# Optimization experiments

Measured on AMD Instinct MI355X. Metric: run time of the kernel, lower is better.

The kernel has to match this reference:

```python
import jax, jax.numpy as jnp
import numpy as np

KERNEL = 3
DILATIONS = (2, 3)
NUM_HEADS = 8


def _unfold_windows(t, k, dil):
    # t: [B, C, H, W] -> [B, C, k*k, H, W], same layout as nn.Unfold(k, dil, pad=dil*(k-1)//2)
    B, C, H, W = t.shape
    pad = dil * (k - 1) // 2
    tp = jnp.pad(t, ((0, 0), (0, 0), (pad, pad), (pad, pad)))
    ws = [tp[:, :, i * dil:i * dil + H, j * dil:j * dil + W]
          for i in range(k) for j in range(k)]
    return jnp.stack(ws, axis=2)


def _dilate_attention(q, k_, v, kernel, dil, head_dim):
    # q,k_,v: [B, d, H, W]
    B, d, H, W = q.shape
    nh = d // head_dim
    scale = head_dim ** (-0.5)
    qh = q.reshape(B, nh, head_dim, H, W)
    kw = _unfold_windows(k_, kernel, dil).reshape(B, nh, head_dim, kernel * kernel, H, W)
    vw = _unfold_windows(v, kernel, dil).reshape(B, nh, head_dim, kernel * kernel, H, W)
    attn = jax.nn.softmax(jnp.einsum('bndhw,bndkhw->bnkhw', qh, kw) * scale, axis=2)
    out = jnp.einsum('bnkhw,bndkhw->bndhw', attn, vw)  # [B, nh, hd, H, W]
    return out.transpose(0, 3, 4, 1, 2).reshape(B, H, W, d)


def setup_inputs() -> dict:
    key = jax.random.key(0)
    k1, k2, k3, k4 = jax.random.split(key, 4)
    B, H, W, C = 4, 128, 128, 256
    x = jax.random.normal(k1, (B, H, W, C), dtype=jnp.float32)
    Wqkv = jax.random.normal(k2, (3 * C, C), dtype=jnp.float32) * (C ** -0.5)
    Wproj = jax.random.normal(k3, (C, C), dtype=jnp.float32) * (C ** -0.5)
    bproj = jnp.zeros((C,), dtype=jnp.float32)
    return {"x": x, "Wqkv": Wqkv, "Wproj": Wproj, "bproj": bproj}


def reference(x, Wqkv, Wproj, bproj):
    B, H, W, C = x.shape
    nd = len(DILATIONS)
    head_dim = C // NUM_HEADS
    # 1x1 conv qkv (no bias), then split into 3 and nd dilation groups
    qkv = jnp.einsum('bhwc,oc->bohw', x, Wqkv).reshape(B, 3, nd, C // nd, H, W)
    outs = []
    for i, dil in enumerate(DILATIONS):
        q, k_, v = qkv[:, 0, i], qkv[:, 1, i], qkv[:, 2, i]
        outs.append(_dilate_attention(q, k_, v, KERNEL, dil, head_dim))
    xo = jnp.concatenate(outs, axis=-1)  # [B, H, W, C], dilation-group-major channels
    return jnp.einsum('bhwc,oc->bhwo', xo, Wproj) + bproj
```

## Files before the change

kernel.cpp:

```cpp
#include <hip/hip_runtime.h>
#include <stdint.h>


typedef __attribute__((ext_vector_type(8))) short bf16x8;
typedef __attribute__((ext_vector_type(4))) float f32x4;

__device__ __forceinline__ void unpack2(unsigned u, float& lo, float& hi) {
  union { unsigned u; float f; } a, b;
  a.u = u << 16;
  b.u = u & 0xffff0000u;
  lo = a.f; hi = b.f;
}
__device__ __forceinline__ unsigned short f2bf(float f) {
  union { float f; unsigned u; } x; x.f = f;
  unsigned r = x.u + 0x7fffu + ((x.u >> 16) & 1u);
  return (unsigned short)(r >> 16);
}
__device__ __forceinline__ unsigned pk2bf(float a, float b) {
  return (unsigned)f2bf(a) | ((unsigned)f2bf(b) << 16);
}

__global__ __launch_bounds__(256) void cvt_f32_to_bf16(
    const float* __restrict__ src, unsigned short* __restrict__ dst, int n) {
  int i = (blockIdx.x * 256 + threadIdx.x) * 8;
  if (i + 8 <= n) {
    const float4* s = (const float4*)(src + i);
    float4 a = s[0], b = s[1];
    uint4 o;
    o.x = pk2bf(a.x, a.y); o.y = pk2bf(a.z, a.w);
    o.z = pk2bf(b.x, b.y); o.w = pk2bf(b.z, b.w);
    *(uint4*)(dst + i) = o;
  } else {
    for (; i < n; ++i) dst[i] = f2bf(src[i]);
  }
}

#define BARX()                                                \
  do {                                                        \
    asm volatile("s_waitcnt lgkmcnt(0)" ::: "memory");        \
    __builtin_amdgcn_s_barrier();                             \
    __builtin_amdgcn_sched_barrier(0);                        \
  } while (0)
#define WAITVM(n)                                             \
  do {                                                        \
    asm volatile("s_waitcnt vmcnt(" #n ")" ::: "memory");     \
    __builtin_amdgcn_sched_barrier(0);                        \
  } while (0)

template <int OUTF32>
__global__ __launch_bounds__(256) void gemm_bt(
    const unsigned short* __restrict__ A, const unsigned short* __restrict__ B,
    void* __restrict__ Cout, const float* __restrict__ bias,
    int N, int NT) {
  __shared__ __align__(16) unsigned short lds[17408];

  const int tid  = threadIdx.x;
  const int lane = tid & 63;
  const int wv   = tid >> 6;
  const int wr   = wv >> 1;
  const int wc   = wv & 1;

  const int nwg = gridDim.x;
  const int q8  = nwg >> 3;
  const int nid = (blockIdx.x & 7) * q8 + (blockIdx.x >> 3);
  const int n0  = (nid % NT) * 128;
  const int m0  = (nid / NT) * 128;

  const int stg_row = wv * 16 + (lane >> 2);
  const int stg_k   = ((lane & 3) ^ ((lane >> 3) & 3)) * 8;
  const unsigned short* Ag = A + (size_t)(m0 + stg_row) * 256 + stg_k;
  const unsigned short* Bg = B + (size_t)(n0 + stg_row) * 256 + stg_k;

  f32x4 acc[4][4];
#pragma unroll
  for (int i = 0; i < 4; ++i)
#pragma unroll
    for (int j = 0; j < 4; ++j) acc[i][j] = (f32x4){0.f, 0.f, 0.f, 0.f};

  const int a_r = lane & 15;

#define STAGE(buf, kt)                                                         \
  do {                                                                         \
    const unsigned short* Asrc = Ag + (kt) * 32;                               \
    const unsigned short* Bsrc = Bg + (kt) * 32;                               \
    _Pragma("unroll")                                                          \
    for (int it = 0; it < 2; ++it) {                                           \
      __builtin_amdgcn_global_load_lds(                                        \
          (const __attribute__((address_space(1))) void*)(Asrc + (size_t)it * 64 * 256), \
          (__attribute__((address_space(3))) void*)&lds[(buf) * 8192 + it * 2048 + wv * 512], \
          16, 0, 0);                                                           \
      __builtin_amdgcn_global_load_lds(                                        \
          (const __attribute__((address_space(1))) void*)(Bsrc + (size_t)it * 64 * 256), \
          (__attribute__((address_space(3))) void*)&lds[(buf) * 8192 + 4096 + it * 2048 + wv * 512], \
          16, 0, 0);                                                           \
    }                                                                          \
  } while (0)

#define COMPUTE(buf)                                                           \
  do {                                                                         \
    const int gsw = (((lane >> 4) ^ ((lane >> 1) & 3))) * 8;                   \
    bf16x8 af[4], bfr[4];                                                      \
    _Pragma("unroll")                                                          \
    for (int mi = 0; mi < 4; ++mi)                                             \
      af[mi] = *(const bf16x8*)&lds[(buf) * 8192 + (wr * 64 + mi * 16 + a_r) * 32 + gsw]; \
    _Pragma("unroll")                                                          \
    for (int ni = 0; ni < 4; ++ni)                                             \
      bfr[ni] = *(const bf16x8*)&lds[(buf) * 8192 + 4096 + (wc * 64 + ni * 16 + a_r) * 32 + gsw]; \
    _Pragma("unroll")                                                          \
    for (int mi = 0; mi < 4; ++mi)                                             \
      _Pragma("unroll")                                                        \
      for (int ni = 0; ni < 4; ++ni)                                           \
        acc[mi][ni] = __builtin_amdgcn_mfma_f32_16x16x32_bf16(                 \
            af[mi], bfr[ni], acc[mi][ni], 0, 0, 0);                            \
  } while (0)

  STAGE(0, 0);
  STAGE(1, 1);
  WAITVM(4);  BARX();
  COMPUTE(0);  BARX();
  STAGE(0, 2); WAITVM(4); BARX();
  COMPUTE(1);  BARX();
  STAGE(1, 3); WAITVM(4); BARX();
  COMPUTE(0);  BARX();
  STAGE(0, 4); WAITVM(4); BARX();
  COMPUTE(1);  BARX();
  STAGE(1, 5); WAITVM(4); BARX();
  COMPUTE(0);  BARX();
  STAGE(0, 6); WAITVM(4); BARX();
  COMPUTE(1);  BARX();
  STAGE(1, 7); WAITVM(4); BARX();
  COMPUTE(0);  BARX();
  WAITVM(0);   BARX();
  COMPUTE(1);  BARX();

  const int cl = wc * 64 + a_r;
  const int rl = wr * 64 + (lane >> 4) * 4;
  if (!OUTF32) {
    unsigned short* eb = &lds[0];
#pragma unroll
    for (int ni = 0; ni < 4; ++ni)
#pragma unroll
      for (int mi = 0; mi < 4; ++mi)
#pragma unroll
        for (int r = 0; r < 4; ++r)
          eb[(rl + mi * 16 + r) * 136 + cl + ni * 16] = f2bf(acc[mi][ni][r]);
    BARX();
    unsigned short* C = (unsigned short*)Cout;
#pragma unroll
    for (int p = 0; p < 8; ++p) {
      const int idx = p * 256 + tid;
      const int row = idx >> 4;
      const int seg = idx & 15;
      uint4 v = *(const uint4*)&eb[row * 136 + seg * 8];
      *(uint4*)&C[(size_t)(m0 + row) * N + n0 + seg * 8] = v;
    }
  } else {
    float* ef = (float*)&lds[0];
    float* C = (float*)Cout;
    float bv[4];
#pragma unroll
    for (int ni = 0; ni < 4; ++ni) bv[ni] = bias[n0 + wc * 64 + ni * 16 + a_r];
#pragma unroll
    for (int half = 0; half < 2; ++half) {
      if (wr == half) {
        const int rb = (lane >> 4) * 4;
#pragma unroll
        for (int ni = 0; ni < 4; ++ni)
#pragma unroll
          for (int mi = 0; mi < 4; ++mi)
#pragma unroll
            for (int r = 0; r < 4; ++r)
              ef[(rb + mi * 16 + r) * 132 + wc * 64 + ni * 16 + a_r] =
                  acc[mi][ni][r] + bv[ni];
      }
      BARX();
#pragma unroll
      for (int p = 0; p < 8; ++p) {
        const int idx = p * 256 + tid;
        const int row = idx >> 5;
        const int seg = idx & 31;
        f32x4 v = *(const f32x4*)&ef[row * 132 + seg * 4];
        *(f32x4*)&C[(size_t)(m0 + half * 64 + row) * N + n0 + seg * 4] = v;
      }
      BARX();
    }
  }
#undef STAGE
#undef COMPUTE
}

__global__ __launch_bounds__(256) void attn_kernel(
    const unsigned short* __restrict__ qkv, unsigned short* __restrict__ xo) {
  const int nwg = gridDim.x;
  const int q8  = nwg >> 3;
  const int bid = (blockIdx.x & 7) * q8 + (blockIdx.x >> 3);
  const int gid   = bid * 256 + threadIdx.x;
  const int combo = gid & 7;
  const int pixel = gid >> 3;
  const int w = pixel & 127;
  const int h = (pixel >> 7) & 127;
  const int b = pixel >> 14;
  const int dil = (combo >> 2) ? 3 : 2;
  const int choff = combo * 32;

  const unsigned short* qp = qkv + (size_t)pixel * 768 + choff;
  float q[32];
#pragma unroll
  for (int t = 0; t < 4; ++t) {
    uint4 u = *(const uint4*)(qp + t * 8);
    unpack2(u.x, q[t * 8 + 0], q[t * 8 + 1]);
    unpack2(u.y, q[t * 8 + 2], q[t * 8 + 3]);
    unpack2(u.z, q[t * 8 + 4], q[t * 8 + 5]);
    unpack2(u.w, q[t * 8 + 6], q[t * 8 + 7]);
  }

  float sc[9];
#pragma unroll
  for (int i = 0; i < 3; ++i) {
#pragma unroll
    for (int j = 0; j < 3; ++j) {
      const int hh = h + (i - 1) * dil;
      const int ww = w + (j - 1) * dil;
      float s = 0.f;
      if ((unsigned)hh < 128u && (unsigned)ww < 128u) {
        const unsigned short* kp =
            qkv + (size_t)((((b << 7) | hh) << 7) | ww) * 768 + 256 + choff;
#pragma unroll
        for (int t = 0; t < 4; ++t) {
          uint4 u = *(const uint4*)(kp + t * 8);
          float a0, a1;
          unpack2(u.x, a0, a1); s += q[t * 8 + 0] * a0 + q[t * 8 + 1] * a1;
          unpack2(u.y, a0, a1); s += q[t * 8 + 2] * a0 + q[t * 8 + 3] * a1;
          unpack2(u.z, a0, a1); s += q[t * 8 + 4] * a0 + q[t * 8 + 5] * a1;
          unpack2(u.w, a0, a1); s += q[t * 8 + 6] * a0 + q[t * 8 + 7] * a1;
        }
      }
      sc[i * 3 + j] = s * 0.17677669529663687f;
    }
  }

  float mx = sc[0];
#pragma unroll
  for (int t = 1; t < 9; ++t) mx = fmaxf(mx, sc[t]);
  float wgt[9], sum = 0.f;
#pragma unroll
  for (int t = 0; t < 9; ++t) { wgt[t] = __expf(sc[t] - mx); sum += wgt[t]; }
  const float inv = 1.f / sum;

  float o[32];
#pragma unroll
  for (int t = 0; t < 32; ++t) o[t] = 0.f;
#pragma unroll
  for (int i = 0; i < 3; ++i) {
#pragma unroll
    for (int j = 0; j < 3; ++j) {
      const int hh = h + (i - 1) * dil;
      const int ww = w + (j - 1) * dil;
      if ((unsigned)hh < 128u && (unsigned)ww < 128u) {
        const float wv = wgt[i * 3 + j] * inv;
        const unsigned short* vp =
            qkv + (size_t)((((b << 7) | hh) << 7) | ww) * 768 + 512 + choff;
#pragma unroll
        for (int t = 0; t < 4; ++t) {
          uint4 u = *(const uint4*)(vp + t * 8);
          float a0, a1;
          unpack2(u.x, a0, a1); o[t * 8 + 0] += wv * a0; o[t * 8 + 1] += wv * a1;
          unpack2(u.y, a0, a1); o[t * 8 + 2] += wv * a0; o[t * 8 + 3] += wv * a1;
          unpack2(u.z, a0, a1); o[t * 8 + 4] += wv * a0; o[t * 8 + 5] += wv * a1;
          unpack2(u.w, a0, a1); o[t * 8 + 6] += wv * a0; o[t * 8 + 7] += wv * a1;
        }
      }
    }
  }

  unsigned short* op = xo + (size_t)pixel * 256 + choff;
#pragma unroll
  for (int t = 0; t < 4; ++t) {
    uint4 u;
    u.x = pk2bf(o[t * 8 + 0], o[t * 8 + 1]);
    u.y = pk2bf(o[t * 8 + 2], o[t * 8 + 3]);
    u.z = pk2bf(o[t * 8 + 4], o[t * 8 + 5]);
    u.w = pk2bf(o[t * 8 + 6], o[t * 8 + 7]);
    *(uint4*)(op + t * 8) = u;
  }
}

extern "C" void kernel_launch(void* const* d_in, const int* in_sizes, int n_in,
                              void* d_out, int out_size, void* d_ws, size_t ws_size,
                              hipStream_t stream) {
  const float* x     = (const float*)d_in[0];
  const float* Wqkv  = (const float*)d_in[1];
  const float* Wproj = (const float*)d_in[2];
  const float* bproj = (const float*)d_in[3];

  const int M = 4 * 128 * 128;
  const int C = 256;

  unsigned short* xb     = (unsigned short*)d_ws;
  unsigned short* qkvb   = xb + (size_t)M * C;
  unsigned short* xob    = qkvb + (size_t)M * 3 * C;
  unsigned short* wqkvb  = xob + (size_t)M * C;
  unsigned short* wprojb = wqkvb + (size_t)3 * C * C;

  cvt_f32_to_bf16<<<(M * C / 8 + 255) / 256, 256, 0, stream>>>(x, xb, M * C);
  cvt_f32_to_bf16<<<(3 * C * C / 8 + 255) / 256, 256, 0, stream>>>(Wqkv, wqkvb, 3 * C * C);
  cvt_f32_to_bf16<<<(C * C / 8 + 255) / 256, 256, 0, stream>>>(Wproj, wprojb, C * C);

  gemm_bt<0><<<(M / 128) * (3 * C / 128), 256, 0, stream>>>(
      xb, wqkvb, (void*)qkvb, nullptr, 3 * C, 3 * C / 128);

  attn_kernel<<<(M * 8) / 256, 256, 0, stream>>>(qkvb, xob);

  gemm_bt<1><<<(M / 128) * (C / 128), 256, 0, stream>>>(
      xob, wprojb, d_out, bproj, C, C / 128);
}
```

Baseline: 130.0 us.

## Tile attention kernel spatially and stage K/V halo in shared memory

The attention kernel now gives each workgroup a 16x16 pixel tile for one head/dilation combo. It cooperatively loads the K and V halo region (22x22 pixels, 8 planes of 8 bf16) into LDS with zero padding, then reads all 9 neighbours from LDS instead of issuing redundant global loads. It also folds the softmax scale into q and uses packed float2 arithmetic. This cuts repeated global/L2 traffic for overlapping windows, at the cost of about 62KB of LDS per block, which limits occupancy, plus a barrier.

```diff
diff --git a/kernel.cpp b/kernel.cpp
--- a/kernel.cpp
+++ b/kernel.cpp
@@ -4,12 +4,13 @@
 
 typedef __attribute__((ext_vector_type(8))) short bf16x8;
 typedef __attribute__((ext_vector_type(4))) float f32x4;
-
-__device__ __forceinline__ void unpack2(unsigned u, float& lo, float& hi) {
+typedef __attribute__((ext_vector_type(2))) float f32x2;
+
+__device__ __forceinline__ f32x2 up2(unsigned u) {
   union { unsigned u; float f; } a, b;
   a.u = u << 16;
   b.u = u & 0xffff0000u;
-  lo = a.f; hi = b.f;
+  return (f32x2){a.f, b.f};
 }
 __device__ __forceinline__ unsigned short f2bf(float f) {
   union { float f; unsigned u; } x; x.f = f;
@@ -191,27 +192,59 @@
 
 __global__ __launch_bounds__(256) void attn_kernel(
     const unsigned short* __restrict__ qkv, unsigned short* __restrict__ xo) {
+  __shared__ __align__(16) unsigned short lds[8 * 485 * 8];
+
   const int nwg = gridDim.x;
   const int q8  = nwg >> 3;
-  const int bid = (blockIdx.x & 7) * q8 + (blockIdx.x >> 3);
-  const int gid   = bid * 256 + threadIdx.x;
-  const int combo = gid & 7;
-  const int pixel = gid >> 3;
-  const int w = pixel & 127;
-  const int h = (pixel >> 7) & 127;
-  const int b = pixel >> 14;
-  const int dil = (combo >> 2) ? 3 : 2;
+  const int nid = (blockIdx.x & 7) * q8 + (blockIdx.x >> 3);
+  const int combo = nid & 7;
+  const int tw    = (nid >> 3) & 7;
+  const int th    = (nid >> 6) & 7;
+  const int b     = nid >> 9;
+  const int d     = (combo >> 2) ? 3 : 2;
   const int choff = combo * 32;
-
-  const unsigned short* qp = qkv + (size_t)pixel * 768 + choff;
-  float q[32];
-#pragma unroll
-  for (int t = 0; t < 4; ++t) {
-    uint4 u = *(const uint4*)(qp + t * 8);
-    unpack2(u.x, q[t * 8 + 0], q[t * 8 + 1]);
-    unpack2(u.y, q[t * 8 + 2], q[t * 8 + 3]);
-    unpack2(u.z, q[t * 8 + 4], q[t * 8 + 5]);
-    unpack2(u.w, q[t * 8 + 6], q[t * 8 + 7]);
+  const int h0 = th * 16, w0 = tw * 16;
+  const int t = threadIdx.x;
+
+#pragma unroll
+  for (int it = 0; it < 16; ++it) {
+    const int slot  = it * 256 + t;
+    const int px    = slot >> 3;
+    const int plane = slot & 7;
+    const int r = px / 22, c = px % 22;
+    const int gh = h0 - d + r;
+    const int gw = w0 - d + c;
+    const bool live = (slot < 3872);
+    const bool ok = live && ((unsigned)gh < 128u) && ((unsigned)gw < 128u);
+    const int hcl = min(max(gh, 0), 127);
+    const int wcl = min(max(gw, 0), 127);
+    const int gp = (((b << 7) | hcl) << 7) | wcl;
+    const unsigned short* src = qkv + (size_t)gp * 768 + 256 +
+                                (plane >> 2) * 256 + (plane & 3) * 8 + choff;
+    uint4 u = *(const uint4*)src;
+    if (!ok) u = make_uint4(0u, 0u, 0u, 0u);
+    if (live) *(uint4*)&lds[(plane * 485 + px) * 8] = u;
+  }
+  __syncthreads();
+
+  const int ph = t >> 4, pw = t & 15;
+  const int gp0 = (((b << 7) | (h0 + ph)) << 7) | (w0 + pw);
+  const unsigned short* qp = qkv + (size_t)gp0 * 768 + choff;
+  f32x2 q2[16];
+  {
+    uint4 u0 = *(const uint4*)qp;
+    uint4 u1 = *(const uint4*)(qp + 8);
+    uint4 u2 = *(const uint4*)(qp + 16);
+    uint4 u3 = *(const uint4*)(qp + 24);
+    const f32x2 s2 = {0.17677669529663687f, 0.17677669529663687f};
+    q2[0]  = up2(u0.x) * s2; q2[1]  = up2(u0.y) * s2;
+    q2[2]  = up2(u0.z) * s2; q2[3]  = up2(u0.w) * s2;
+    q2[4]  = up2(u1.x) * s2; q2[5]  = up2(u1.y) * s2;
+    q2[6]  = up2(u1.z) * s2; q2[7]  = up2(u1.w) * s2;
+    q2[8]  = up2(u2.x) * s2; q2[9]  = up2(u2.y) * s2;
+    q2[10] = up2(u2.z) * s2; q2[11] = up2(u2.w) * s2;
+    q2[12] = up2(u3.x) * s2; q2[13] = up2(u3.y) * s2;
+    q2[14] = up2(u3.z) * s2; q2[15] = up2(u3.w) * s2;
   }
 
   float sc[9];
@@ -219,70 +252,71 @@
   for (int i = 0; i < 3; ++i) {
 #pragma unroll
     for (int j = 0; j < 3; ++j) {
-      const int hh = h + (i - 1) * dil;
-      const int ww = w + (j - 1) * dil;
-      float s = 0.f;
-      if ((unsigned)hh < 128u && (unsigned)ww < 128u) {
-        const unsigned short* kp =
-            qkv + (size_t)((((b << 7) | hh) << 7) | ww) * 768 + 256 + choff;
-#pragma unroll
-        for (int t = 0; t < 4; ++t) {
-          uint4 u = *(const uint4*)(kp + t * 8);
-          float a0, a1;
-          unpack2(u.x, a0, a1); s += q[t * 8 + 0] * a0 + q[t * 8 + 1] * a1;
-          unpack2(u.y, a0, a1); s += q[t * 8 + 2] * a0 + q[t * 8 + 3] * a1;
-          unpack2(u.z, a0, a1); s += q[t * 8 + 4] * a0 + q[t * 8 + 5] * a1;
-          unpack2(u.w, a0, a1); s += q[t * 8 + 6] * a0 + q[t * 8 + 7] * a1;
-        }
-      }
-      sc[i * 3 + j] = s * 0.17677669529663687f;
+      const int lp = (ph + i * d) * 22 + (pw + j * d);
+      const uint4 k0 = *(const uint4*)&lds[(0 * 485 + lp) * 8];
+      const uint4 k1 = *(const uint4*)&lds[(1 * 485 + lp) * 8];
+      const uint4 k2 = *(const uint4*)&lds[(2 * 485 + lp) * 8];
+      const uint4 k3 = *(const uint4*)&lds[(3 * 485 + lp) * 8];
+      f32x2 p0 = q2[0] * up2(k0.x);
+      p0 += q2[1] * up2(k0.y); p0 += q2[2] * up2(k0.z); p0 += q2[3] * up2(k0.w);
+      f32x2 p1 = q2[4] * up2(k1.x);
+      p1 += q2[5] * up2(k1.y); p1 += q2[6] * up2(k1.z); p1 += q2[7] * up2(k1.w);
+      f32x2 p2 = q2[8] * up2(k2.x);
+      p2 += q2[9] * up2(k2.y); p2 += q2[10] * up2(k2.z); p2 += q2[11] * up2(k2.w);
+      f32x2 p3 = q2[12] * up2(k3.x);
+      p3 += q2[13] * up2(k3.y); p3 += q2[14] * up2(k3.z); p3 += q2[15] * up2(k3.w);
+      const f32x2 s = (p0 + p1) + (p2 + p3);
+      sc[i * 3 + j] = s.x + s.y;
     }
   }
 
   float mx = sc[0];
 #pragma unroll
-  for (int t = 1; t < 9; ++t) mx = fmaxf(mx, sc[t]);
-  float wgt[9], sum = 0.f;
-#pragma unroll
-  for (int t = 0; t < 9; ++t) { wgt[t] = __expf(sc[t] - mx); sum += wgt[t]; }
+  for (int k = 1; k < 9; ++k) mx = fmaxf(mx, sc[k]);
+  float sum = 0.f;
+#pragma unroll
+  for (int k = 0; k < 9; ++k) { sc[k] = __expf(sc[k] - mx); sum += sc[k]; }
   const float inv = 1.f / sum;
 
-  float o[32];
-#pragma unroll
-  for (int t = 0; t < 32; ++t) o[t] = 0.f;
+  f32x2 o2[16];
+#pragma unroll
+  for (int k = 0; k < 16; ++k) o2[k] = (f32x2){0.f, 0.f};
 #pragma unroll
   for (int i = 0; i < 3; ++i) {
 #pragma unroll
     for (int j = 0; j < 3; ++j) {
-      const int hh = h + (i - 1) * dil;
-      const int ww = w + (j - 1) * dil;
-      if ((unsigned)hh < 128u && (unsigned)ww < 128u) {
-        const float wv = wgt[i * 3 + j] * inv;
-        const unsigned short* vp =
-            qkv + (size_t)((((b << 7) | hh) << 7) | ww) * 768 + 512 + choff;
-#pragma unroll
-        for (int t = 0; t < 4; ++t) {
-          uint4 u = *(const uint4*)(vp + t * 8);
-          float a0, a1;
-          unpack2(u.x, a0, a1); o[t * 8 + 0] += wv * a0; o[t * 8 + 1] += wv * a1;
-          unpack2(u.y, a0, a1); o[t * 8 + 2] += wv * a0; o[t * 8 + 3] += wv * a1;
-          unpack2(u.z, a0, a1); o[t * 8 + 4] += wv * a0; o[t * 8 + 5] += wv * a1;
-          unpack2(u.w, a0, a1); o[t * 8 + 6] += wv * a0; o[t * 8 + 7] += wv * a1;
-        }
-      }
+      const int lp = (ph + i * d) * 22 + (pw + j * d);
+      const uint4 v0 = *(const uint4*)&lds[(4 * 485 + lp) * 8];
+      const uint4 v1 = *(const uint4*)&lds[(5 * 485 + lp) * 8];
+      const uint4 v2 = *(const uint4*)&lds[(6 * 485 + lp) * 8];
+      const uint4 v3 = *(const uint4*)&lds[(7 * 485 + lp) * 8];
+      const float wv = sc[i * 3 + j] * inv;
+      const f32x2 w2 = {wv, wv};
+      o2[0]  += w2 * up2(v0.x); o2[1]  += w2 * up2(v0.y);
+      o2[2]  += w2 * up2(v0.z); o2[3]  += w2 * up2(v0.w);
+      o2[4]  += w2 * up2(v1.x); o2[5]  += w2 * up2(v1.y);
+      o2[6]  += w2 * up2(v1.z); o2[7]  += w2 * up2(v1.w);
+      o2[8]  += w2 * up2(v2.x); o2[9]  += w2 * up2(v2.y);
+      o2[10] += w2 * up2(v2.z); o2[11] += w2 * up2(v2.w);
+      o2[12] += w2 * up2(v3.x); o2[13] += w2 * up2(v3.y);
+      o2[14] += w2 * up2(v3.z); o2[15] += w2 * up2(v3.w);
     }
   }
 
-  unsigned short* op = xo + (size_t)pixel * 256 + choff;
-#pragma unroll
-  for (int t = 0; t < 4; ++t) {
-    uint4 u;
-    u.x = pk2bf(o[t * 8 + 0], o[t * 8 + 1]);
-    u.y = pk2bf(o[t * 8 + 2], o[t * 8 + 3]);
-    u.z = pk2bf(o[t * 8 + 4], o[t * 8 + 5]);
-    u.w = pk2bf(o[t * 8 + 6], o[t * 8 + 7]);
-    *(uint4*)(op + t * 8) = u;
-  }
+  unsigned short* op = xo + (size_t)gp0 * 256 + choff;
+  uint4 s0, s1, s2o, s3o;
+  s0.x  = pk2bf(o2[0].x,  o2[0].y);  s0.y  = pk2bf(o2[1].x,  o2[1].y);
+  s0.z  = pk2bf(o2[2].x,  o2[2].y);  s0.w  = pk2bf(o2[3].x,  o2[3].y);
+  s1.x  = pk2bf(o2[4].x,  o2[4].y);  s1.y  = pk2bf(o2[5].x,  o2[5].y);
+  s1.z  = pk2bf(o2[6].x,  o2[6].y);  s1.w  = pk2bf(o2[7].x,  o2[7].y);
+  s2o.x = pk2bf(o2[8].x,  o2[8].y);  s2o.y = pk2bf(o2[9].x,  o2[9].y);
+  s2o.z = pk2bf(o2[10].x, o2[10].y); s2o.w = pk2bf(o2[11].x, o2[11].y);
+  s3o.x = pk2bf(o2[12].x, o2[12].y); s3o.y = pk2bf(o2[13].x, o2[13].y);
+  s3o.z = pk2bf(o2[14].x, o2[14].y); s3o.w = pk2bf(o2[15].x, o2[15].y);
+  *(uint4*)op        = s0;
+  *(uint4*)(op + 8)  = s1;
+  *(uint4*)(op + 16) = s2o;
+  *(uint4*)(op + 24) = s3o;
 }
 
 extern "C" void kernel_launch(void* const* d_in, const int* in_sizes, int n_in,
@@ -309,7 +343,7 @@
   gemm_bt<0><<<(M / 128) * (3 * C / 128), 256, 0, stream>>>(
       xb, wqkvb, (void*)qkvb, nullptr, 3 * C, 3 * C / 128);
 
-  attn_kernel<<<(M * 8) / 256, 256, 0, stream>>>(qkvb, xob);
+  attn_kernel<<<2048, 256, 0, stream>>>(qkvb, xob);
 
   gemm_bt<1><<<(M / 128) * (C / 128), 256, 0, stream>>>(
       xob, wprojb, d_out, bproj, C, C / 128);
```

Result: faster. 126.8 us (-2.4%).
